# Performance work log

Measured on AMD Instinct MI355X. Metric: run time of the kernel, lower is better.

The kernel has to match this reference:

```python
import jax, jax.numpy as jnp
import numpy as np

V = 100000   # vertices
C = 64       # in channels
D = 64       # out channels
W = 8        # weight matrices
DEG = 16     # neighbors per vertex
E = V * DEG  # edges


def setup_inputs() -> dict:
    key = jax.random.key(0)
    k = jax.random.split(key, 6)
    data = jax.random.normal(k[0], (V, C), dtype=jnp.float32)
    # fixed-degree adjacency: vertex i has DEG neighbors (arbitrary dst)
    edge_src = jnp.repeat(jnp.arange(V, dtype=jnp.int32), DEG)        # [E] sorted
    edge_dst = jax.random.randint(k[1], (E,), 0, V, dtype=jnp.int32)  # [E]
    edge_vals = jnp.full((E,), 1.0 / DEG, dtype=jnp.float32)          # row-normalized
    var_u = 0.1 * jax.random.normal(k[2], (C, W), dtype=jnp.float32)
    var_c = 0.1 * jax.random.normal(k[3], (W,), dtype=jnp.float32)
    var_w = 0.1 * jax.random.normal(k[4], (W, C, D), dtype=jnp.float32)
    var_b = 0.1 * jax.random.normal(k[5], (D,), dtype=jnp.float32)
    return {"data": data, "edge_src": edge_src, "edge_dst": edge_dst,
            "edge_vals": edge_vals, "var_u": var_u, "var_c": var_c,
            "var_w": var_w, "var_b": var_b}


def reference(data, edge_src, edge_dst, edge_vals, var_u, var_c, var_w, var_b):
    # translation_invariant=True => var_v = -var_u
    num_v = data.shape[0]
    x_u = data @ var_u            # [V, W]
    x_v = data @ (-var_u)         # [V, W]
    # edge logits and exp-normalize over the W weight matrices (softmax == exp/sum)
    logits = x_u[edge_src] + x_v[edge_dst] + var_c   # [E, W]
    q = jax.nn.softmax(logits, axis=-1)              # [E, W]
    # gathered neighbor features, pre-scaled by adjacency values
    x_sep = data[edge_dst] * edge_vals[:, None]      # [E, C]
    y = jnp.zeros((num_v, var_w.shape[-1]), dtype=data.dtype)
    for m in range(var_c.shape[0]):  # small fixed loop over W weight matrices
        agg = jax.ops.segment_sum(q[:, m:m + 1] * x_sep, edge_src,
                                  num_segments=num_v)  # [V, C]
        y = y + agg @ var_w[m]                          # [V, D]
    return y + var_b
```

## Files before the change

kernel.cpp:

```cpp
#include <hip/hip_runtime.h>

typedef _Float16 half2_t __attribute__((ext_vector_type(2)));
typedef _Float16 half4_t __attribute__((ext_vector_type(4)));
typedef _Float16 half8_t __attribute__((ext_vector_type(8)));
typedef __attribute__((ext_vector_type(4))) float f32x4;

#define NV 100000
#define NTILE 6250
#define GRID 512
#define LDSZ 81920

#define VMWAIT(N) asm volatile("s_waitcnt vmcnt(" #N ")" ::: "memory")
#define LGKM0     asm volatile("s_waitcnt lgkmcnt(0)" ::: "memory")
#define FENCE     asm volatile("" ::: "memory")

__device__ __forceinline__ unsigned cvt_pk_u(float a, float b) {
  auto h = __builtin_amdgcn_cvt_pkrtz(a, b);
  return __builtin_bit_cast(unsigned, h);
}
__device__ __forceinline__ half2_t u2h(unsigned u) { return __builtin_bit_cast(half2_t, u); }
__device__ __forceinline__ unsigned lds_off(const void* p) {
  return (unsigned)(size_t)(const __attribute__((address_space(3))) char*)p;
}
__device__ __forceinline__ void load16_to_lds(const void* g, void* s) {
  __builtin_amdgcn_global_load_lds(
      (const __attribute__((address_space(1))) unsigned int*)g,
      (__attribute__((address_space(3))) unsigned int*)s, 16, 0, 0);
}

__global__ __launch_bounds__(256) void k0_prep_w(const float* __restrict__ var_w,
                                                 unsigned short* __restrict__ Bt) {
  int t = blockIdx.x * 256 + threadIdx.x;
  if (t >= 64 * 512) return;
  int d = t >> 9, k = t & 511;
  _Float16 h = (_Float16)var_w[k * 64 + d];
  Bt[t] = __builtin_bit_cast(unsigned short, h);
}

__global__ __launch_bounds__(256) void k1_prep(const float* __restrict__ data,
                                               const float* __restrict__ var_u,
                                               unsigned short* __restrict__ data_h,
                                               unsigned short* __restrict__ xu_h) {
  __shared__ float u_lds[512];
  int tid = threadIdx.x;
  u_lds[tid] = var_u[tid];
  u_lds[tid + 256] = var_u[tid + 256];
  __syncthreads();
  int v = blockIdx.x * 256 + tid;
  if (v >= NV) return;
  const float4* dp = (const float4*)(data + v * 64);
  float acc[8];
#pragma unroll
  for (int w = 0; w < 8; ++w) acc[w] = 0.f;
  uint4* ob = (uint4*)(data_h + v * 64);
#pragma unroll
  for (int q = 0; q < 8; ++q) {
    float4 a4 = dp[q * 2], b4 = dp[q * 2 + 1];
    int c0 = q * 8;
#pragma unroll
    for (int w = 0; w < 8; ++w)
      acc[w] += a4.x * u_lds[(c0 + 0) * 8 + w] + a4.y * u_lds[(c0 + 1) * 8 + w]
              + a4.z * u_lds[(c0 + 2) * 8 + w] + a4.w * u_lds[(c0 + 3) * 8 + w]
              + b4.x * u_lds[(c0 + 4) * 8 + w] + b4.y * u_lds[(c0 + 5) * 8 + w]
              + b4.z * u_lds[(c0 + 6) * 8 + w] + b4.w * u_lds[(c0 + 7) * 8 + w];
    uint4 pk;
    pk.x = cvt_pk_u(a4.x, a4.y); pk.y = cvt_pk_u(a4.z, a4.w);
    pk.z = cvt_pk_u(b4.x, b4.y); pk.w = cvt_pk_u(b4.z, b4.w);
    ob[q] = pk;
  }
  uint4 xp;
  xp.x = cvt_pk_u(acc[0], acc[1]); xp.y = cvt_pk_u(acc[2], acc[3]);
  xp.z = cvt_pk_u(acc[4], acc[5]); xp.w = cvt_pk_u(acc[6], acc[7]);
  *(uint4*)(xu_h + v * 8) = xp;
}

__global__ __launch_bounds__(256, 2) void k2_main(
    const unsigned short* __restrict__ data_h,
    const unsigned short* __restrict__ xu_h,
    const int* __restrict__ edge_dst,
    const float* __restrict__ edge_vals,
    const unsigned short* __restrict__ Bt,
    const float* __restrict__ var_c,
    const float* __restrict__ var_b,
    float* __restrict__ y) {
  extern __shared__ __align__(16) char smem[];
  char* XB0  = smem;
  char* XUD0 = smem + 65536;
  char* LIN0 = smem + 73728;

  int tid = threadIdx.x;
  int wave = tid >> 6;
  int l = tid & 63;
  int q4 = l >> 4;
  int row = l & 15;
  int col = row + wave * 16;

  uint4 btf[16];
#pragma unroll
  for (int ks = 0; ks < 16; ++ks)
    btf[ks] = *(const uint4*)(Bt + (col * 512 + ks * 32 + q4 * 8));
  float c8[8];
#pragma unroll
  for (int m = 0; m < 8; ++m) c8[m] = var_c[m];
  float bias = var_b[col];

#define LIN_DMA(SL, TS)                                                        \
  { char* lb_ = LIN0 + (SL) * 2048;                                            \
    if ((wave & 1) == 0)                                                       \
      load16_to_lds(edge_dst + (size_t)(TS) * 256 + l * 4, lb_);               \
    else                                                                       \
      load16_to_lds(edge_vals + (size_t)(TS) * 256 + l * 4, lb_ + 1024); }
#define XUD_DMA(SL, LSL)                                                       \
  { const int* ld_ = (const int*)(LIN0 + (LSL) * 2048);                        \
    int dv_ = ld_[wave * 64 + l];                                              \
    load16_to_lds(xu_h + (size_t)dv_ * 8, XUD0 + (SL) * 4096 + wave * 1024); }
#define X_DMA(SL, LSL)                                                         \
  { const int* ld_ = (const int*)(LIN0 + (LSL) * 2048);                        \
    int j_ = ((l >> 3) & 3) * 4 + ((l >> 1) & 3);                              \
    int ch0_ = ((l >> 5) << 1) | (l & 1);                                      \
    _Pragma("unroll")                                                          \
    for (int s_ = 0; s_ < 8; ++s_) {                                           \
      int dv_ = ld_[wave * 64 + (s_ >> 1) * 16 + j_];                          \
      int ch_ = ch0_ + (s_ & 1) * 4;                                           \
      load16_to_lds(data_h + (size_t)dv_ * 64 + ch_ * 8,                       \
                    XB0 + (SL) * 32768 + wave * 8192 + s_ * 1024); } }

  int t0 = blockIdx.x;
  int tG1 = (t0 + GRID < NTILE) ? t0 + GRID : t0;
  int tG2 = (t0 + 2 * GRID < NTILE) ? t0 + 2 * GRID : t0;
  FENCE;
  LIN_DMA(0, t0);
  LIN_DMA(1, tG1);
  LIN_DMA(2, tG2);
  FENCE;
  uint4 xsA = *(const uint4*)(xu_h + ((size_t)t0 * 16 + wave * 4 + q4) * 8);
  uint4 xsB = *(const uint4*)(xu_h + ((size_t)tG1 * 16 + wave * 4 + q4) * 8);
  VMWAIT(0);
  __builtin_amdgcn_s_barrier();
  FENCE;
  XUD_DMA(0, 0);
  X_DMA(0, 0);
  FENCE;
  VMWAIT(0);
  __builtin_amdgcn_s_barrier();

  int kc = 0;
  for (int t = t0; t < NTILE; t += GRID, ++kc) {
    int slc = kc & 1, lslc = kc & 3;
    int sl1 = (kc + 1) & 1, lsl1 = (kc + 1) & 3, lsl3 = (kc + 3) & 3;
    int t2c = (t + 2 * GRID < NTILE) ? t + 2 * GRID : t;
    int t3c = (t + 3 * GRID < NTILE) ? t + 3 * GRID : t;
    char* XBt = XB0 + slc * 32768;
    char* XUDt = XUD0 + slc * 4096;
    const char* LINt = LIN0 + lslc * 2048;

    FENCE;
    XUD_DMA(sl1, lsl1);
    X_DMA(sl1, lsl1);
    FENCE;

    {
      uint4 xd4 = *(const uint4*)(XUDt + (wave * 64 + l) * 16);
      float evv = ((const float*)(LINt + 1024))[wave * 64 + l];
      half2_t xm01 = u2h(xsA.x), xm23 = u2h(xsA.y), xm45 = u2h(xsA.z), xm67 = u2h(xsA.w);
      half2_t xd01 = u2h(xd4.x), xd23 = u2h(xd4.y), xd45 = u2h(xd4.z), xd67 = u2h(xd4.w);
      float ex0 = __expf((float)xm01[0] - (float)xd01[0] + c8[0]);
      float ex1 = __expf((float)xm01[1] - (float)xd01[1] + c8[1]);
      float ex2 = __expf((float)xm23[0] - (float)xd23[0] + c8[2]);
      float ex3 = __expf((float)xm23[1] - (float)xd23[1] + c8[3]);
      float ex4 = __expf((float)xm45[0] - (float)xd45[0] + c8[4]);
      float ex5 = __expf((float)xm45[1] - (float)xd45[1] + c8[5]);
      float ex6 = __expf((float)xm67[0] - (float)xd67[0] + c8[6]);
      float ex7 = __expf((float)xm67[1] - (float)xd67[1] + c8[7]);
      float ssum = ((ex0 + ex1) + (ex2 + ex3)) + ((ex4 + ex5) + (ex6 + ex7));
      float rs = __builtin_amdgcn_rcpf(ssum) * evv;
      uint4 qq;
      qq.x = cvt_pk_u(ex0 * rs, ex1 * rs);
      qq.y = cvt_pk_u(ex2 * rs, ex3 * rs);
      qq.z = cvt_pk_u(ex4 * rs, ex5 * rs);
      qq.w = cvt_pk_u(ex6 * rs, ex7 * rs);
      int vv = l >> 4, jq = (l >> 2) & 3, jl = l & 3;
      char* qb = XUDt + wave * 1024 + vv * 256;
#pragma unroll
      for (int m = 0; m < 8; ++m) {
        unsigned short hv = (unsigned short)((&qq.x)[m >> 1] >> ((m & 1) * 16));
        int byte = (((m ^ vv) & 7) << 5) + (((jq ^ vv ^ m) & 3) << 3) + jl * 2;
        *(unsigned short*)(qb + byte) = hv;
      }
    }

    uint4 xsC = *(const uint4*)(xu_h + ((size_t)t2c * 16 + wave * 4 + q4) * 8);
    FENCE;
    LIN_DMA(lsl3, t3c);
    FENCE;

    {
      uint2 qfr[4];
#pragma unroll
      for (int vv = 0; vv < 4; ++vv) {
        int srow = (row ^ vv) & 7;
        int gsl = (q4 ^ vv ^ row) & 3;
        qfr[vv] = *(const uint2*)(XUDt + wave * 1024 + vv * 256 + srow * 32 + gsl * 8);
      }
      unsigned xbase = lds_off(XBt + wave * 8192) + l * 8;
      uint2 trd[16];
#pragma unroll
      for (int vv = 0; vv < 4; ++vv)
#pragma unroll
        for (int cb = 0; cb < 4; ++cb) {
          unsigned a_ = xbase + vv * 2048 + cb * 512;
          asm volatile("ds_read_b64_tr_b16 %0, %1"
                       : "=v"(trd[vv * 4 + cb]) : "v"(a_) : "memory");
        }
      LGKM0;
      __builtin_amdgcn_sched_barrier(0);
      f32x4 D[16];
#pragma unroll
      for (int vv = 0; vv < 4; ++vv)
#pragma unroll
        for (int cb = 0; cb < 4; ++cb) {
          f32x4 z = {0.f, 0.f, 0.f, 0.f};
          D[vv * 4 + cb] = __builtin_amdgcn_mfma_f32_16x16x16f16(
              __builtin_bit_cast(half4_t, trd[vv * 4 + cb]),
              __builtin_bit_cast(half4_t, qfr[vv]), z, 0, 0, 0);
        }
      if (row < 8) {
#pragma unroll
        for (int vv = 0; vv < 4; ++vv) {
          int vg = wave * 4 + vv;
          char* ab = XBt + vg * 2048;
#pragma unroll
          for (int cb = 0; cb < 4; ++cb) {
            f32x4 d4 = D[vv * 4 + cb];
            uint2 w2;
            w2.x = cvt_pk_u(d4[0], d4[1]);
            w2.y = cvt_pk_u(d4[2], d4[3]);
            int byte = (row * 128 + cb * 32 + q4 * 8) ^ ((vg & 7) << 4)
                       ^ ((row & 3) << 5);
            *(uint2*)(ab + byte) = w2;
          }
        }
      }
    }
    LGKM0;
    __builtin_amdgcn_s_barrier();

    {
      f32x4 C = {0.f, 0.f, 0.f, 0.f};
#pragma unroll
      for (int ks = 0; ks < 16; ++ks) {
        int bo = (ks * 64 + q4 * 16) ^ ((row & 7) << 4) ^ (((ks >> 1) & 3) << 5);
        half8_t af = *(const half8_t*)(XBt + row * 2048 + bo);
        C = __builtin_amdgcn_mfma_f32_16x16x32_f16(
            af, __builtin_bit_cast(half8_t, btf[ks]), C, 0, 0, 0);
      }
#pragma unroll
      for (int i = 0; i < 4; ++i)
        y[(size_t)(t * 16 + q4 * 4 + i) * 64 + col] = C[i] + bias;
    }
    LGKM0;
    VMWAIT(4);
    __builtin_amdgcn_s_barrier();

    xsA = xsB; xsB = xsC;
  }
  VMWAIT(0);
#undef LIN_DMA
#undef XUD_DMA
#undef X_DMA
}

extern "C" void kernel_launch(void* const* d_in, const int* in_sizes, int n_in,
                              void* d_out, int out_size, void* d_ws, size_t ws_size,
                              hipStream_t stream) {
  const float* data      = (const float*)d_in[0];
  const int*   edge_dst  = (const int*)d_in[2];
  const float* edge_vals = (const float*)d_in[3];
  const float* var_u     = (const float*)d_in[4];
  const float* var_c     = (const float*)d_in[5];
  const float* var_w     = (const float*)d_in[6];
  const float* var_b     = (const float*)d_in[7];
  float* y = (float*)d_out;

  char* ws = (char*)d_ws;
  unsigned short* data_h = (unsigned short*)ws;
  unsigned short* xu_h   = (unsigned short*)(ws + 12800000);
  unsigned short* Bt     = (unsigned short*)(ws + 14400000);

  hipFuncSetAttribute((const void*)k2_main,
                      hipFuncAttributeMaxDynamicSharedMemorySize, LDSZ);

  hipLaunchKernelGGL(k0_prep_w, dim3(128), dim3(256), 0, stream, var_w, Bt);
  hipLaunchKernelGGL(k1_prep, dim3((NV + 255) / 256), dim3(256), 0, stream,
                     data, var_u, data_h, xu_h);
  hipLaunchKernelGGL(k2_main, dim3(GRID), dim3(256), LDSZ, stream,
                     data_h, xu_h, edge_dst, edge_vals, Bt, var_c, var_b, y);
}
```

Measured before the change: 76.26 us.

## Single-buffer LDS with register-prefetched indices to raise occupancy and grid

```diff
diff --git a/kernel.cpp b/kernel.cpp
--- a/kernel.cpp
+++ b/kernel.cpp
@@ -7,8 +7,8 @@
 
 #define NV 100000
 #define NTILE 6250
-#define GRID 512
-#define LDSZ 81920
+#define GRID 768
+#define LDSZ 53248
 
 #define VMWAIT(N) asm volatile("s_waitcnt vmcnt(" #N ")" ::: "memory")
 #define LGKM0     asm volatile("s_waitcnt lgkmcnt(0)" ::: "memory")
@@ -84,9 +84,9 @@
     const float* __restrict__ var_b,
     float* __restrict__ y) {
   extern __shared__ __align__(16) char smem[];
-  char* XB0  = smem;
-  char* XUD0 = smem + 65536;
-  char* LIN0 = smem + 73728;
+  char* XB  = smem;
+  char* AGG = smem + 32768;
+  char* QB  = smem + 49152;
 
   int tid = threadIdx.x;
   int wave = tid >> 6;
@@ -94,6 +94,8 @@
   int q4 = l >> 4;
   int row = l & 15;
   int col = row + wave * 16;
+  int j_ = ((l >> 3) & 3) * 4 + ((l >> 1) & 3);
+  int ch0_ = ((l >> 5) << 1) | (l & 1);
 
   uint4 btf[16];
 #pragma unroll
@@ -104,66 +106,53 @@
   for (int m = 0; m < 8; ++m) c8[m] = var_c[m];
   float bias = var_b[col];
 
-#define LIN_DMA(SL, TS)                                                        \
-  { char* lb_ = LIN0 + (SL) * 2048;                                            \
-    if ((wave & 1) == 0)                                                       \
-      load16_to_lds(edge_dst + (size_t)(TS) * 256 + l * 4, lb_);               \
-    else                                                                       \
-      load16_to_lds(edge_vals + (size_t)(TS) * 256 + l * 4, lb_ + 1024); }
-#define XUD_DMA(SL, LSL)                                                       \
-  { const int* ld_ = (const int*)(LIN0 + (LSL) * 2048);                        \
-    int dv_ = ld_[wave * 64 + l];                                              \
-    load16_to_lds(xu_h + (size_t)dv_ * 8, XUD0 + (SL) * 4096 + wave * 1024); }
-#define X_DMA(SL, LSL)                                                         \
-  { const int* ld_ = (const int*)(LIN0 + (LSL) * 2048);                        \
-    int j_ = ((l >> 3) & 3) * 4 + ((l >> 1) & 3);                              \
-    int ch0_ = ((l >> 5) << 1) | (l & 1);                                      \
-    _Pragma("unroll")                                                          \
-    for (int s_ = 0; s_ < 8; ++s_) {                                           \
-      int dv_ = ld_[wave * 64 + (s_ >> 1) * 16 + j_];                          \
-      int ch_ = ch0_ + (s_ & 1) * 4;                                           \
-      load16_to_lds(data_h + (size_t)dv_ * 64 + ch_ * 8,                       \
-                    XB0 + (SL) * 32768 + wave * 8192 + s_ * 1024); } }
-
   int t0 = blockIdx.x;
   int tG1 = (t0 + GRID < NTILE) ? t0 + GRID : t0;
-  int tG2 = (t0 + 2 * GRID < NTILE) ? t0 + 2 * GRID : t0;
-  FENCE;
-  LIN_DMA(0, t0);
-  LIN_DMA(1, tG1);
-  LIN_DMA(2, tG2);
-  FENCE;
+
   uint4 xsA = *(const uint4*)(xu_h + ((size_t)t0 * 16 + wave * 4 + q4) * 8);
   uint4 xsB = *(const uint4*)(xu_h + ((size_t)tG1 * 16 + wave * 4 + q4) * 8);
+  int dstE_A = edge_dst[(size_t)t0 * 256 + wave * 64 + l];
+  int dstE_B = edge_dst[(size_t)tG1 * 256 + wave * 64 + l];
+  float evA = edge_vals[(size_t)t0 * 256 + wave * 64 + l];
+  uint4 xdA = *(const uint4*)(xu_h + (size_t)dstE_A * 8);
+  int dstXA[4];
+  {
+    int dstX0[4];
+#pragma unroll
+    for (int k = 0; k < 4; ++k) {
+      dstX0[k] = edge_dst[(size_t)t0 * 256 + wave * 64 + k * 16 + j_];
+      dstXA[k] = edge_dst[(size_t)tG1 * 256 + wave * 64 + k * 16 + j_];
+    }
+    FENCE;
+#pragma unroll
+    for (int s_ = 0; s_ < 8; ++s_) {
+      int dv_ = dstX0[s_ >> 1];
+      int ch_ = ch0_ + (s_ & 1) * 4;
+      load16_to_lds(data_h + (size_t)dv_ * 64 + ch_ * 8,
+                    XB + wave * 8192 + s_ * 1024);
+    }
+    FENCE;
+  }
   VMWAIT(0);
   __builtin_amdgcn_s_barrier();
-  FENCE;
-  XUD_DMA(0, 0);
-  X_DMA(0, 0);
-  FENCE;
-  VMWAIT(0);
-  __builtin_amdgcn_s_barrier();
-
-  int kc = 0;
-  for (int t = t0; t < NTILE; t += GRID, ++kc) {
-    int slc = kc & 1, lslc = kc & 3;
-    int sl1 = (kc + 1) & 1, lsl1 = (kc + 1) & 3, lsl3 = (kc + 3) & 3;
+
+  for (int t = t0; t < NTILE; t += GRID) {
+    int t1c = (t + GRID < NTILE) ? t + GRID : t;
     int t2c = (t + 2 * GRID < NTILE) ? t + 2 * GRID : t;
-    int t3c = (t + 3 * GRID < NTILE) ? t + 3 * GRID : t;
-    char* XBt = XB0 + slc * 32768;
-    char* XUDt = XUD0 + slc * 4096;
-    const char* LINt = LIN0 + lslc * 2048;
-
+
+    float evB = edge_vals[(size_t)t1c * 256 + wave * 64 + l];
+    uint4 xdB = *(const uint4*)(xu_h + (size_t)dstE_B * 8);
+    int dstE_C = edge_dst[(size_t)t2c * 256 + wave * 64 + l];
+    uint4 xsC = *(const uint4*)(xu_h + ((size_t)t2c * 16 + wave * 4 + q4) * 8);
+    int dstXB[4];
+#pragma unroll
+    for (int k = 0; k < 4; ++k)
+      dstXB[k] = edge_dst[(size_t)t2c * 256 + wave * 64 + k * 16 + j_];
     FENCE;
-    XUD_DMA(sl1, lsl1);
-    X_DMA(sl1, lsl1);
-    FENCE;
 
     {
-      uint4 xd4 = *(const uint4*)(XUDt + (wave * 64 + l) * 16);
-      float evv = ((const float*)(LINt + 1024))[wave * 64 + l];
       half2_t xm01 = u2h(xsA.x), xm23 = u2h(xsA.y), xm45 = u2h(xsA.z), xm67 = u2h(xsA.w);
-      half2_t xd01 = u2h(xd4.x), xd23 = u2h(xd4.y), xd45 = u2h(xd4.z), xd67 = u2h(xd4.w);
+      half2_t xd01 = u2h(xdA.x), xd23 = u2h(xdA.y), xd45 = u2h(xdA.z), xd67 = u2h(xdA.w);
       float ex0 = __expf((float)xm01[0] - (float)xd01[0] + c8[0]);
       float ex1 = __expf((float)xm01[1] - (float)xd01[1] + c8[1]);
       float ex2 = __expf((float)xm23[0] - (float)xd23[0] + c8[2]);
@@ -173,14 +162,14 @@
       float ex6 = __expf((float)xm67[0] - (float)xd67[0] + c8[6]);
       float ex7 = __expf((float)xm67[1] - (float)xd67[1] + c8[7]);
       float ssum = ((ex0 + ex1) + (ex2 + ex3)) + ((ex4 + ex5) + (ex6 + ex7));
-      float rs = __builtin_amdgcn_rcpf(ssum) * evv;
+      float rs = __builtin_amdgcn_rcpf(ssum) * evA;
       uint4 qq;
       qq.x = cvt_pk_u(ex0 * rs, ex1 * rs);
       qq.y = cvt_pk_u(ex2 * rs, ex3 * rs);
       qq.z = cvt_pk_u(ex4 * rs, ex5 * rs);
       qq.w = cvt_pk_u(ex6 * rs, ex7 * rs);
       int vv = l >> 4, jq = (l >> 2) & 3, jl = l & 3;
-      char* qb = XUDt + wave * 1024 + vv * 256;
+      char* qb = QB + wave * 1024 + vv * 256;
 #pragma unroll
       for (int m = 0; m < 8; ++m) {
         unsigned short hv = (unsigned short)((&qq.x)[m >> 1] >> ((m & 1) * 16));
@@ -189,20 +178,16 @@
       }
     }
 
-    uint4 xsC = *(const uint4*)(xu_h + ((size_t)t2c * 16 + wave * 4 + q4) * 8);
-    FENCE;
-    LIN_DMA(lsl3, t3c);
-    FENCE;
-
     {
       uint2 qfr[4];
 #pragma unroll
       for (int vv = 0; vv < 4; ++vv) {
         int srow = (row ^ vv) & 7;
         int gsl = (q4 ^ vv ^ row) & 3;
-        qfr[vv] = *(const uint2*)(XUDt + wave * 1024 + vv * 256 + srow * 32 + gsl * 8);
-      }
-      unsigned xbase = lds_off(XBt + wave * 8192) + l * 8;
+        qfr[vv] = *(const uint2*)(QB + wave * 1024 + vv * 256 + srow * 32 + gsl * 8);
+      }
+      VMWAIT(12);
+      unsigned xbase = lds_off(XB + wave * 8192) + l * 8;
       uint2 trd[16];
 #pragma unroll
       for (int vv = 0; vv < 4; ++vv)
@@ -213,6 +198,15 @@
                        : "=v"(trd[vv * 4 + cb]) : "v"(a_) : "memory");
         }
       LGKM0;
+      FENCE;
+#pragma unroll
+      for (int s_ = 0; s_ < 8; ++s_) {
+        int dv_ = dstXA[s_ >> 1];
+        int ch_ = ch0_ + (s_ & 1) * 4;
+        load16_to_lds(data_h + (size_t)dv_ * 64 + ch_ * 8,
+                      XB + wave * 8192 + s_ * 1024);
+      }
+      FENCE;
       __builtin_amdgcn_sched_barrier(0);
       f32x4 D[16];
 #pragma unroll
@@ -228,7 +222,7 @@
 #pragma unroll
         for (int vv = 0; vv < 4; ++vv) {
           int vg = wave * 4 + vv;
-          char* ab = XBt + vg * 2048;
+          char* ab = AGG + vg * 1024;
 #pragma unroll
           for (int cb = 0; cb < 4; ++cb) {
             f32x4 d4 = D[vv * 4 + cb];
@@ -250,7 +244,7 @@
 #pragma unroll
       for (int ks = 0; ks < 16; ++ks) {
         int bo = (ks * 64 + q4 * 16) ^ ((row & 7) << 4) ^ (((ks >> 1) & 3) << 5);
-        half8_t af = *(const half8_t*)(XBt + row * 2048 + bo);
+        half8_t af = *(const half8_t*)(AGG + row * 1024 + bo);
         C = __builtin_amdgcn_mfma_f32_16x16x32_f16(
             af, __builtin_bit_cast(half8_t, btf[ks]), C, 0, 0, 0);
       }
@@ -259,15 +253,14 @@
         y[(size_t)(t * 16 + q4 * 4 + i) * 64 + col] = C[i] + bias;
     }
     LGKM0;
-    VMWAIT(4);
     __builtin_amdgcn_s_barrier();
 
     xsA = xsB; xsB = xsC;
+    evA = evB; xdA = xdB; dstE_B = dstE_C;
+#pragma unroll
+    for (int k = 0; k < 4; ++k) dstXA[k] = dstXB[k];
   }
   VMWAIT(0);
-#undef LIN_DMA
-#undef XUD_DMA
-#undef X_DMA
 }
 
 extern "C" void kernel_launch(void* const* d_in, const int* in_sizes, int n_in,
```

Result: slower. 80.65 us (+5.8%).
